# Kernel optimization log

Measured on AMD Instinct MI355X. Metric: run time of the kernel, lower is better.

## Reference

```python
import jax, jax.numpy as jnp
import numpy as np

D_MODEL = 1024
NUM_HEADS = 16
HEAD_DIM = D_MODEL // NUM_HEADS
B, L = 4, 4096


def _linear(x, w, b):
    # torch nn.Linear: y = x @ w.T + b, w: [out, in]
    return jnp.einsum('bld,od->blo', x, w) + b


def _elu_feature_map(x):
    return jax.nn.elu(x) + 1.0


def setup_inputs() -> dict:
    key = jax.random.key(0)
    ks = jax.random.split(key, 11)
    s = 1.0 / np.sqrt(D_MODEL)
    inp = {
        'query': jax.random.normal(ks[0], (B, L, D_MODEL), jnp.float32),
        'key': jax.random.normal(ks[1], (B, L, D_MODEL), jnp.float32),
        'value': jax.random.normal(ks[2], (B, L, D_MODEL), jnp.float32),
        'wq': jax.random.uniform(ks[3], (D_MODEL, D_MODEL), jnp.float32, -s, s),
        'bq': jax.random.uniform(ks[4], (D_MODEL,), jnp.float32, -s, s),
        'wk': jax.random.uniform(ks[5], (D_MODEL, D_MODEL), jnp.float32, -s, s),
        'bk': jax.random.uniform(ks[6], (D_MODEL,), jnp.float32, -s, s),
        'wv': jax.random.uniform(ks[7], (D_MODEL, D_MODEL), jnp.float32, -s, s),
        'bv': jax.random.uniform(ks[8], (D_MODEL,), jnp.float32, -s, s),
        'wo': jax.random.uniform(ks[9], (D_MODEL, D_MODEL), jnp.float32, -s, s),
        'bo': jax.random.uniform(ks[10], (D_MODEL,), jnp.float32, -s, s),
    }
    return inp


def reference(query, key, value, wq, bq, wk, bk, wv, bv, wo, bo):
    Bsz, Lq, _ = query.shape
    # project and split heads -> [B, H, L, hd]
    def split_heads(x):
        return x.reshape(Bsz, -1, NUM_HEADS, HEAD_DIM).transpose(0, 2, 1, 3)
    Q = split_heads(_linear(query, wq, bq))
    K = split_heads(_linear(key, wk, bk))
    V = split_heads(_linear(value, wv, bv))
    Q = _elu_feature_map(Q)
    K = _elu_feature_map(K)
    # KV: [B, H, hd, hd]
    KV = jnp.einsum('bhld,bhle->bhde', K, V)
    Ksum = K.sum(axis=2)  # [B, H, hd]
    Z = 1.0 / (jnp.einsum('bhld,bhd->bhl', Q, Ksum) + 1e-6)  # [B, H, Lq]
    out = jnp.einsum('bhld,bhde->bhle', Q, KV) * Z[..., None]
    out = out.transpose(0, 2, 1, 3).reshape(Bsz, Lq, D_MODEL)
    return _linear(out, wo, bo)
```

## Files before the change

kernel.cpp:

```cpp
#include <hip/hip_runtime.h>
#include <hip/hip_bf16.h>

typedef _Float16 half8 __attribute__((ext_vector_type(8)));
typedef _Float16 half4 __attribute__((ext_vector_type(4)));
typedef float f32x4 __attribute__((ext_vector_type(4)));

#define KDIM 1024
#define NDIM 1024
#define MROWS 16384

#define GLD_LDS16(g, l)                                                  \
  __builtin_amdgcn_global_load_lds(                                      \
      (const __attribute__((address_space(1))) void*)(g),                \
      (__attribute__((address_space(3))) void*)(l), 16, 0, 0)

__global__ __launch_bounds__(256)
void cvt_in(const float* __restrict__ s0, _Float16* __restrict__ d0,
            const float* __restrict__ s1, _Float16* __restrict__ d1,
            const float* __restrict__ s2, _Float16* __restrict__ d2) {
  const float* src;
  _Float16* dst;
  switch (blockIdx.y) {
    case 0: src = s0; dst = d0; break;
    case 1: src = s1; dst = d1; break;
    default: src = s2; dst = d2; break;
  }
  size_t i = (size_t)blockIdx.x * 256 + threadIdx.x;
  float4 f = ((const float4*)src)[i];
  half4 h;
  h[0] = (_Float16)f.x; h[1] = (_Float16)f.y;
  h[2] = (_Float16)f.z; h[3] = (_Float16)f.w;
  ((half4*)dst)[i] = h;
}

__global__ __launch_bounds__(256)
void cvt_w(const float* __restrict__ s0, _Float16* __restrict__ d0,
           const float* __restrict__ s1, _Float16* __restrict__ d1,
           const float* __restrict__ s2, _Float16* __restrict__ d2,
           const float* __restrict__ s3, _Float16* __restrict__ d3) {
  const float* src;
  _Float16* dst;
  switch (blockIdx.y) {
    case 0: src = s0; dst = d0; break;
    case 1: src = s1; dst = d1; break;
    case 2: src = s2; dst = d2; break;
    default: src = s3; dst = d3; break;
  }
  size_t i = (size_t)blockIdx.x * 256 + threadIdx.x;
  float4 f = ((const float4*)src)[i];
  half4 h;
  h[0] = (_Float16)f.x; h[1] = (_Float16)f.y;
  h[2] = (_Float16)f.z; h[3] = (_Float16)f.w;
  ((half4*)dst)[i] = h;
}

template <int ACT, int TRANS, int FUSE, typename TOUT>
__global__ __launch_bounds__(512, 2)
void gemm_bk32(const _Float16* __restrict__ X, const _Float16* __restrict__ W,
               const float* __restrict__ bias, TOUT* __restrict__ Y,
               const _Float16* __restrict__ KVTx) {
  constexpr int BM = 256, BN = 128, BK = 32;
  __shared__ char smem[73728];
  _Float16* As = (_Float16*)smem;
  _Float16* Bs = (_Float16*)(smem + 49152);

  const int tid  = threadIdx.x;
  const int lane = tid & 63;
  const int w    = tid >> 6;
  const int wm   = w >> 1;
  const int wn   = w & 1;

  const int bid = blockIdx.x;
  const int wid = (bid & 7) * 64 + (bid >> 3);
  const int m0  = (wid >> 3) * BM;
  const int n0  = (wid & 7) * BN;

  const int lrw = lane >> 2;
  const int gsl = (lane & 3) ^ (lrw & 3);
  const _Float16* gA = X + (size_t)(m0 + w * 16 + lrw) * KDIM + gsl * 8;
  const _Float16* gB = W + (size_t)(n0 + w * 16 + lrw) * KDIM + gsl * 8;

#define STAGE32(kt, bidx)                                                     \
  {                                                                           \
    const int k0s = (kt) * BK;                                                \
    _Float16* la = As + (bidx) * (BM * BK) + (w * 16) * BK;                   \
    _Float16* lb = Bs + (bidx) * (BN * BK) + (w * 16) * BK;                   \
    GLD_LDS16(gA + k0s, la);                                                  \
    GLD_LDS16(gA + (size_t)128 * KDIM + k0s, la + 128 * BK);                  \
    GLD_LDS16(gB + k0s, lb);                                                  \
  }

  const int rsl = ((lane >> 4) ^ (lane & 3)) << 4;

  f32x4 acc[4][4] = {};

  STAGE32(0, 0);
  STAGE32(1, 1);
  asm volatile("s_waitcnt vmcnt(3)" ::: "memory");
  asm volatile("s_barrier" ::: "memory");

  int bc = 0;
  for (int t = 0; t < 32; ++t) {
    int bs = bc + 2; if (bs >= 3) bs -= 3;
    const char* Ab = (const char*)As + bc * (BM * BK * 2);
    const char* Bb = (const char*)Bs + bc * (BN * BK * 2);

    half8 afr[4], bfr[4];
#pragma unroll
    for (int mi = 0; mi < 4; ++mi) {
      int row = wm * 64 + mi * 16 + (lane & 15);
      afr[mi] = *(const half8*)(Ab + row * 64 + rsl);
    }
#pragma unroll
    for (int ni = 0; ni < 4; ++ni) {
      int row = wn * 64 + ni * 16 + (lane & 15);
      bfr[ni] = *(const half8*)(Bb + row * 64 + rsl);
    }

    if (t < 30) STAGE32(t + 2, bs);

    __builtin_amdgcn_s_setprio(1);
#pragma unroll
    for (int mi = 0; mi < 4; ++mi)
#pragma unroll
      for (int ni = 0; ni < 4; ++ni)
        acc[mi][ni] = __builtin_amdgcn_mfma_f32_16x16x32_f16(
            afr[mi], bfr[ni], acc[mi][ni], 0, 0, 0);
    __builtin_amdgcn_s_setprio(0);

    if (t < 30) {
      asm volatile("s_waitcnt vmcnt(3)" ::: "memory");
      asm volatile("s_barrier" ::: "memory");
    } else if (t == 30) {
      asm volatile("s_waitcnt vmcnt(0)" ::: "memory");
      asm volatile("s_barrier" ::: "memory");
    }
    ++bc; if (bc == 3) bc = 0;
  }
#undef STAGE32

  if constexpr (FUSE) {
    __syncthreads();
    _Float16* Ct = (_Float16*)smem;
#pragma unroll
    for (int ni = 0; ni < 4; ++ni) {
      int cl   = wn * 64 + ni * 16 + (lane & 15);
      float bv = bias[n0 + cl];
#pragma unroll
      for (int mi = 0; mi < 4; ++mi) {
#pragma unroll
        for (int i = 0; i < 4; ++i) {
          int row = wm * 64 + mi * 16 + ((lane >> 4) << 2) + i;
          float v = acc[mi][ni][i] + bv;
          v = (v > 0.f) ? (v + 1.f) : __expf(v);
          int byte = row * 256 + cl * 2;
          byte ^= (row & 7) << 4;
          *(_Float16*)((char*)Ct + byte) = (_Float16)v;
        }
      }
    }
    __syncthreads();
    const int bh0 = ((m0 >> 12) << 4) + (n0 >> 6);
    const _Float16* kvp = KVTx + (size_t)(bh0 + wn) * 5120;
    f32x4 acc2[4][5] = {};
#pragma unroll
    for (int kk = 0; kk < 2; ++kk) {
      half8 afr2[4], bfr2[5];
#pragma unroll
      for (int m = 0; m < 4; ++m) {
        int row  = wm * 64 + m * 16 + (lane & 15);
        int byte = row * 256 + wn * 128 + kk * 64 + ((lane >> 4) << 4);
        byte ^= (row & 7) << 4;
        afr2[m] = *(const half8*)((const char*)Ct + byte);
      }
#pragma unroll
      for (int n = 0; n < 5; ++n) {
        int row = n * 16 + (lane & 15);
        bfr2[n] = *(const half8*)(kvp + row * 64 + kk * 32 + ((lane >> 4) << 3));
      }
#pragma unroll
      for (int m = 0; m < 4; ++m)
#pragma unroll
        for (int n = 0; n < 5; ++n)
          acc2[m][n] = __builtin_amdgcn_mfma_f32_16x16x32_f16(
              afr2[m], bfr2[n], acc2[m][n], 0, 0, 0);
    }
#pragma unroll
    for (int m = 0; m < 4; ++m) {
#pragma unroll
      for (int i = 0; i < 4; ++i) {
        float dn = __shfl(acc2[m][4][i], lane & 48);
        float z  = 1.f / (dn + 1e-6f);
        size_t row = (size_t)m0 + wm * 64 + m * 16 + ((lane >> 4) << 2) + i;
#pragma unroll
        for (int n = 0; n < 4; ++n) {
          int col = n0 + wn * 64 + n * 16 + (lane & 15);
          Y[row * NDIM + col] = (TOUT)(acc2[m][n][i] * z);
        }
      }
    }
    return;
  }

#pragma unroll
  for (int ni = 0; ni < 4; ++ni) {
    int col  = n0 + wn * 64 + ni * 16 + (lane & 15);
    float bv = bias[col];
#pragma unroll
    for (int mi = 0; mi < 4; ++mi) {
      int r0 = m0 + wm * 64 + mi * 16 + ((lane >> 4) << 2);
      if constexpr (TRANS) {
        int b  = r0 >> 12;
        int l0 = r0 & 4095;
        half4 hv;
#pragma unroll
        for (int i = 0; i < 4; ++i) {
          float v = acc[mi][ni][i] + bv;
          if constexpr (ACT == 1) v = (v > 0.f) ? (v + 1.f) : __expf(v);
          hv[i] = (_Float16)v;
        }
        *(half4*)((_Float16*)Y + ((size_t)(b * 1024 + col)) * 4096 + l0) = hv;
      } else {
#pragma unroll
        for (int i = 0; i < 4; ++i) {
          float v = acc[mi][ni][i] + bv;
          if constexpr (ACT == 1) v = (v > 0.f) ? (v + 1.f) : __expf(v);
          Y[(size_t)(r0 + i) * NDIM + col] = (TOUT)v;
        }
      }
    }
  }
}

__global__ __launch_bounds__(256, 2)
void kv_mfma(const _Float16* __restrict__ KT, const _Float16* __restrict__ VT,
             _Float16* __restrict__ pKV) {
  const int bh = blockIdx.x;
  const int ch = blockIdx.y;
  const int tid  = threadIdx.x;
  const int lane = tid & 63;
  const int w    = tid >> 6;

  __shared__ _Float16 As[64 * 64];
  __shared__ _Float16 Bs[64 * 64];

  const int lr = lane >> 3;
  const int ls = (lane & 7) ^ lr;
  const size_t lbase = (size_t)ch * 1024 + ls * 8;
  const _Float16* gA = VT + (size_t)(bh * 64 + w * 16 + lr) * 4096 + lbase;
  const _Float16* gB = KT + (size_t)(bh * 64 + w * 16 + lr) * 4096 + lbase;
  _Float16* ldsA = As + (w * 16) * 64;
  _Float16* ldsB = Bs + (w * 16) * 64;

  half8 aones;
#pragma unroll
  for (int j = 0; j < 8; ++j) aones[j] = (lane & 15) == 0 ? (_Float16)1.0f : (_Float16)0.0f;

  f32x4 acc[5] = {};

  for (int k0 = 0; k0 < 1024; k0 += 64) {
    __syncthreads();
#pragma unroll
    for (int c = 0; c < 2; ++c) {
      GLD_LDS16(gA + k0 + (size_t)(c * 8) * 4096, ldsA + c * 8 * 64);
      GLD_LDS16(gB + k0 + (size_t)(c * 8) * 4096, ldsB + c * 8 * 64);
    }
    __syncthreads();

    half8 afr[4][2], bfr[2];
#pragma unroll
    for (int m = 0; m < 4; ++m)
#pragma unroll
      for (int kk = 0; kk < 2; ++kk) {
        int row  = m * 16 + (lane & 15);
        int byte = row * 128 + ((lane >> 4) << 4) + kk * 64;
        byte ^= (row & 7) << 4;
        afr[m][kk] = *(const half8*)((const char*)As + byte);
      }
#pragma unroll
    for (int kk = 0; kk < 2; ++kk) {
      int row  = w * 16 + (lane & 15);
      int byte = row * 128 + ((lane >> 4) << 4) + kk * 64;
      byte ^= (row & 7) << 4;
      bfr[kk] = *(const half8*)((const char*)Bs + byte);
    }
#pragma unroll
    for (int kk = 0; kk < 2; ++kk) {
#pragma unroll
      for (int m = 0; m < 4; ++m)
        acc[m] = __builtin_amdgcn_mfma_f32_16x16x32_f16(afr[m][kk], bfr[kk],
                                                        acc[m], 0, 0, 0);
      acc[4] = __builtin_amdgcn_mfma_f32_16x16x32_f16(aones, bfr[kk],
                                                      acc[4], 0, 0, 0);
    }
  }

  _Float16* outp = pKV + ((size_t)ch * 64 + bh) * 5120;
  const int col = w * 16 + (lane & 15);
#pragma unroll
  for (int m = 0; m < 5; ++m) {
#pragma unroll
    for (int i = 0; i < 4; ++i) {
      int row = m * 16 + ((lane >> 4) << 2) + i;
      outp[row * 64 + col] = (_Float16)acc[m][i];
    }
  }
}

__global__ __launch_bounds__(256)
void kv_combine(const _Float16* __restrict__ pKV, _Float16* __restrict__ KVTx) {
  int g = blockIdx.x * 256 + threadIdx.x;
  int bh = g / 5120;
  int j  = g - bh * 5120;
  float s = 0.f;
#pragma unroll
  for (int ch = 0; ch < 4; ++ch)
    s += (float)pKV[((size_t)ch * 64 + bh) * 5120 + j];
  KVTx[(size_t)bh * 5120 + j] = (_Float16)s;
}

extern "C" void kernel_launch(void* const* d_in, const int* in_sizes, int n_in,
                              void* d_out, int out_size, void* d_ws, size_t ws_size,
                              hipStream_t stream) {
  const float* q  = (const float*)d_in[0];
  const float* k  = (const float*)d_in[1];
  const float* v  = (const float*)d_in[2];
  const float* wq = (const float*)d_in[3];
  const float* bq = (const float*)d_in[4];
  const float* wk = (const float*)d_in[5];
  const float* bk = (const float*)d_in[6];
  const float* wv = (const float*)d_in[7];
  const float* bv = (const float*)d_in[8];
  const float* wo = (const float*)d_in[9];
  const float* bo = (const float*)d_in[10];
  float* out = (float*)d_out;

  char* ws = (char*)d_ws;
  _Float16* Xq   = (_Float16*)(ws);
  _Float16* KT   = (_Float16*)(ws + 33554432);
  _Float16* VT   = (_Float16*)(ws + 67108864);
  _Float16* pKV  = (_Float16*)(ws + 100663296);
  _Float16* whk  = (_Float16*)(ws + 100663296);
  _Float16* whv  = (_Float16*)(ws + 102760448);
  _Float16* whq  = (_Float16*)(ws + 104857600);
  _Float16* who  = (_Float16*)(ws + 106954752);
  _Float16* att  = KT;
  _Float16* Xk   = (_Float16*)d_out;
  _Float16* Xv   = (_Float16*)((char*)d_out + 33554432);
  _Float16* KVTx = (_Float16*)((char*)d_out + 33554432);

  const int GBLK = (MROWS / 256) * (NDIM / 128);

  cvt_w<<<dim3(1024, 4), 256, 0, stream>>>(wq, whq, wk, whk, wv, whv, wo, who);
  cvt_in<<<dim3(16384, 3), 256, 0, stream>>>(k, Xk, v, Xv, q, Xq);

  gemm_bk32<1, 1, 0, _Float16><<<GBLK, 512, 0, stream>>>(Xk, whk, bk, KT, nullptr);
  gemm_bk32<0, 1, 0, _Float16><<<GBLK, 512, 0, stream>>>(Xv, whv, bv, VT, nullptr);

  kv_mfma<<<dim3(64, 4), 256, 0, stream>>>(KT, VT, pKV);
  kv_combine<<<1280, 256, 0, stream>>>(pKV, KVTx);

  gemm_bk32<1, 0, 1, _Float16><<<GBLK, 512, 0, stream>>>(Xq, whq, bq, att, KVTx);

  gemm_bk32<0, 0, 0, float><<<GBLK, 512, 0, stream>>>(att, who, bo, out, nullptr);
}
```

Baseline: 262.8 us.

## Convert each input to fp16 just before its GEMM and change LDS swizzle

Replaces the single three-input conversion kernel with a grid-stride fp32-to-fp16 converter that writes 8 halves per thread. It is launched separately before each projection GEMM into one shared workspace buffer, so the fp16 copy is likely still in cache when the GEMM reads it. KVTx moves out of the output buffer into the workspace. The LDS XOR swizzle for the A/B tile loads and reads is also changed, to reduce bank conflicts. The cost is two extra kernel launches, and the new swizzle must stay consistent between the store and load sides.

```diff
diff --git a/kernel.cpp b/kernel.cpp
--- a/kernel.cpp
+++ b/kernel.cpp
@@ -15,22 +15,18 @@
       (__attribute__((address_space(3))) void*)(l), 16, 0, 0)
 
 __global__ __launch_bounds__(256)
-void cvt_in(const float* __restrict__ s0, _Float16* __restrict__ d0,
-            const float* __restrict__ s1, _Float16* __restrict__ d1,
-            const float* __restrict__ s2, _Float16* __restrict__ d2) {
-  const float* src;
-  _Float16* dst;
-  switch (blockIdx.y) {
-    case 0: src = s0; dst = d0; break;
-    case 1: src = s1; dst = d1; break;
-    default: src = s2; dst = d2; break;
-  }
-  size_t i = (size_t)blockIdx.x * 256 + threadIdx.x;
-  float4 f = ((const float4*)src)[i];
-  half4 h;
-  h[0] = (_Float16)f.x; h[1] = (_Float16)f.y;
-  h[2] = (_Float16)f.z; h[3] = (_Float16)f.w;
-  ((half4*)dst)[i] = h;
+void cvt_f32_to_f16(const float* __restrict__ src, _Float16* __restrict__ dst,
+                    int n8) {
+  for (int i = blockIdx.x * 256 + threadIdx.x; i < n8; i += gridDim.x * 256) {
+    float4 f0 = ((const float4*)src)[2 * i];
+    float4 f1 = ((const float4*)src)[2 * i + 1];
+    half8 h;
+    h[0] = (_Float16)f0.x; h[1] = (_Float16)f0.y;
+    h[2] = (_Float16)f0.z; h[3] = (_Float16)f0.w;
+    h[4] = (_Float16)f1.x; h[5] = (_Float16)f1.y;
+    h[6] = (_Float16)f1.z; h[7] = (_Float16)f1.w;
+    ((half8*)dst)[i] = h;
+  }
 }
 
 __global__ __launch_bounds__(256)
@@ -76,7 +72,7 @@
   const int n0  = (wid & 7) * BN;
 
   const int lrw = lane >> 2;
-  const int gsl = (lane & 3) ^ (lrw & 3);
+  const int gsl = (lane & 3) ^ ((lane >> 3) & 3);
   const _Float16* gA = X + (size_t)(m0 + w * 16 + lrw) * KDIM + gsl * 8;
   const _Float16* gB = W + (size_t)(n0 + w * 16 + lrw) * KDIM + gsl * 8;
 
@@ -90,7 +86,7 @@
     GLD_LDS16(gB + k0s, lb);                                                  \
   }
 
-  const int rsl = ((lane >> 4) ^ (lane & 3)) << 4;
+  const int rsl = ((lane >> 4) ^ ((lane >> 1) & 3)) << 4;
 
   f32x4 acc[4][4] = {};
 
@@ -336,7 +332,7 @@
   float* out = (float*)d_out;
 
   char* ws = (char*)d_ws;
-  _Float16* Xq   = (_Float16*)(ws);
+  _Float16* Xh   = (_Float16*)(ws);
   _Float16* KT   = (_Float16*)(ws + 33554432);
   _Float16* VT   = (_Float16*)(ws + 67108864);
   _Float16* pKV  = (_Float16*)(ws + 100663296);
@@ -344,23 +340,24 @@
   _Float16* whv  = (_Float16*)(ws + 102760448);
   _Float16* whq  = (_Float16*)(ws + 104857600);
   _Float16* who  = (_Float16*)(ws + 106954752);
+  _Float16* KVTx = (_Float16*)(ws + 109051904);
   _Float16* att  = KT;
-  _Float16* Xk   = (_Float16*)d_out;
-  _Float16* Xv   = (_Float16*)((char*)d_out + 33554432);
-  _Float16* KVTx = (_Float16*)((char*)d_out + 33554432);
-
+
+  const int N8_BIG = MROWS * KDIM / 8;
   const int GBLK = (MROWS / 256) * (NDIM / 128);
 
   cvt_w<<<dim3(1024, 4), 256, 0, stream>>>(wq, whq, wk, whk, wv, whv, wo, who);
-  cvt_in<<<dim3(16384, 3), 256, 0, stream>>>(k, Xk, v, Xv, q, Xq);
-
-  gemm_bk32<1, 1, 0, _Float16><<<GBLK, 512, 0, stream>>>(Xk, whk, bk, KT, nullptr);
-  gemm_bk32<0, 1, 0, _Float16><<<GBLK, 512, 0, stream>>>(Xv, whv, bv, VT, nullptr);
+
+  cvt_f32_to_f16<<<2048, 256, 0, stream>>>(k, Xh, N8_BIG);
+  gemm_bk32<1, 1, 0, _Float16><<<GBLK, 512, 0, stream>>>(Xh, whk, bk, KT, nullptr);
+  cvt_f32_to_f16<<<2048, 256, 0, stream>>>(v, Xh, N8_BIG);
+  gemm_bk32<0, 1, 0, _Float16><<<GBLK, 512, 0, stream>>>(Xh, whv, bv, VT, nullptr);
 
   kv_mfma<<<dim3(64, 4), 256, 0, stream>>>(KT, VT, pKV);
   kv_combine<<<1280, 256, 0, stream>>>(pKV, KVTx);
 
-  gemm_bk32<1, 0, 1, _Float16><<<GBLK, 512, 0, stream>>>(Xq, whq, bq, att, KVTx);
+  cvt_f32_to_f16<<<2048, 256, 0, stream>>>(q, Xh, N8_BIG);
+  gemm_bk32<1, 0, 1, _Float16><<<GBLK, 512, 0, stream>>>(Xh, whq, bq, att, KVTx);
 
   gemm_bk32<0, 0, 0, float><<<GBLK, 512, 0, stream>>>(att, who, bo, out, nullptr);
 }
```

After: 262.4 us. About the same (-0.1%).
